# Kernel tuning notes

Hardware: AMD Instinct MI355X
Metric: run time of the kernel (lower is better)

## Reference

```python
import jax, jax.numpy as jnp
import numpy as np

B, L, D = 128, 50, 128
NUM_NODE, S, HOP = 100000, 12, 2
ALPHA = 0.2      # leaky-relu slope in local aggregator (opt.alpha)
T = 1.0          # softmax temperature (opt.t)
NEG_INF = -9e15


def setup_inputs() -> dict:
    key = jax.random.key(0)
    ks = jax.random.split(key, 13)
    stdv = 1.0 / np.sqrt(D)
    u = lambda k, shape: jax.random.uniform(k, shape, jnp.float32, -stdv, stdv)
    return {
        "inputs": jax.random.randint(ks[0], (B, L), 0, NUM_NODE),
        "adj": jax.random.randint(ks[1], (B, L, L), 0, 5),          # edge types 0..4
        "mask_item": jnp.ones((B, L), dtype=jnp.int32),
        "item": jax.random.randint(ks[2], (B, L), 0, NUM_NODE),
        "emb": u(ks[3], (NUM_NODE, D)),                              # item embedding table
        "adj_all": jax.random.randint(ks[4], (NUM_NODE, S), 0, NUM_NODE),  # global neighbor table
        "num_w": jax.random.uniform(ks[5], (NUM_NODE, S), jnp.float32, 0.0, 10.0),  # co-occur weights
        "a0": u(ks[6], (D,)), "a1": u(ks[7], (D,)), "a2": u(ks[8], (D,)), "a3": u(ks[9], (D,)),
        "gw1": u(ks[10], (HOP, D + 1, D)),   # GlobalAggregator w_1 per hop
        "gw2": u(ks[11], (HOP, D)),          # GlobalAggregator w_2 per hop
        "gw3": u(ks[12], (HOP, 2 * D, D)),   # GlobalAggregator w_3 per hop
    }


def reference(inputs, adj, mask_item, item, emb, adj_all, num_w,
              a0, a1, a2, a3, gw1, gw2, gw3):
    h = emb[inputs]                                   # [B,L,D]

    # ---- LocalAggregator: 4 edge-type GAT over session graph ----
    a_input = h[:, :, None, :] * h[:, None, :, :]     # [B,L,L,D] pairwise hadamard
    def edge_logits(a):
        return jax.nn.leaky_relu(jnp.einsum('bijd,d->bij', a_input, a), ALPHA)
    e = [edge_logits(a) for a in (a0, a1, a2, a3)]
    logits = jnp.full_like(e[0], NEG_INF)
    for k in range(4):
        logits = jnp.where(adj == k + 1, e[k], logits)
    attn = jax.nn.softmax(logits, axis=-1)
    h_local = jnp.einsum('bij,bjd->bid', attn, h)     # [B,L,D]

    # ---- multi-hop neighbor sampling (pure gathers) ----
    item_neighbors = [inputs]
    weight_neighbors = []
    for _ in range(HOP):
        flat = item_neighbors[-1].reshape(-1)
        item_neighbors.append(adj_all[flat].reshape(B, -1))
        weight_neighbors.append(num_w[flat].reshape(B, -1))
    entity = [emb[idx] for idx in item_neighbors]     # hop h: [B, L*S^h, D]

    # ---- session-mean representation ----
    mf = mask_item.astype(jnp.float32)
    sum_item = (emb[item] * mf[..., None]).sum(1) / mf.sum(-1, keepdims=True)  # [B,D]

    # ---- GlobalAggregator: weighted neighbor attention, hop-by-hop ----
    for n_hop in range(HOP):
        nxt = []
        for hp in range(HOP - n_hop):
            sv = entity[hp]                               # [B,M,D]
            nv = entity[hp + 1].reshape(B, -1, S, D)      # [B,M,S,D]
            nw = weight_neighbors[hp].reshape(B, -1, S)   # [B,M,S]
            a = jnp.concatenate([sum_item[:, None, None, :] * nv, nw[..., None]], -1)  # [B,M,S,D+1]
            a = jax.nn.leaky_relu(jnp.einsum('bmsk,kd->bmsd', a, gw1[n_hop]), 0.2)
            a = jnp.einsum('bmsd,d->bms', a, gw2[n_hop]) / T
            attn_g = jax.nn.softmax(a, axis=-1)[..., None]
            nv_agg = (attn_g * nv).sum(-2)                # [B,M,D]
            out = jnp.concatenate([sv, nv_agg], -1) @ gw3[n_hop]
            out = jnp.maximum(out, 0.0)                   # opt.activate == 'relu'
            nxt.append(out)
        entity = nxt
    s_global = entity[0]                                  # [B,L,D]

    # dropout omitted (eval mode)
    output = h_local + s_global
    return output, s_global
```

## Files before the change

kernel.cpp:

```cpp
#include <hip/hip_runtime.h>
#include <hip/hip_bf16.h>
#include <math.h>

#define B_ 128
#define L_ 50
#define D_ 128
#define S_ 12
#define NEG_INF_ -9e15f

typedef __attribute__((ext_vector_type(8))) _Float16 half8;
typedef __attribute__((ext_vector_type(4))) float f32x4;

static __device__ __forceinline__ float lrelu(float x){ return fmaxf(x, 0.2f*x); }
static __device__ __forceinline__ float fexp(float x){ return __expf(x); }
static __device__ __forceinline__ float frcp(float x){ return __builtin_amdgcn_rcpf(x); }

__global__ __launch_bounds__(256) void local_agg_kernel(
    const int* __restrict__ inputs, const int* __restrict__ adj,
    const float* __restrict__ emb,
    const float* __restrict__ a0, const float* __restrict__ a1,
    const float* __restrict__ a2, const float* __restrict__ a3,
    float* __restrict__ hlocal_out)
{
  __shared__ float hs[L_][129];
  __shared__ float alds[4][129];
  __shared__ float att[13][51];
  const int b = blockIdx.x, tid = threadIdx.x;
  const int r0 = blockIdx.y * 13;
  const int nr = (L_ - r0) < 13 ? (L_ - r0) : 13;

  if (tid < 128){
    alds[0][tid] = a0[tid]; alds[1][tid] = a1[tid];
    alds[2][tid] = a2[tid]; alds[3][tid] = a3[tid];
  }
  for (int i = tid; i < L_*D_; i += 256){
    int r = i >> 7, d = i & 127;
    hs[r][d] = emb[(size_t)inputs[b*L_ + r]*D_ + d];
  }
  __syncthreads();

  for (int pth = tid; pth < nr*L_; pth += 256){
    int i = pth / L_, j = pth % L_;
    int at = adj[b*L_*L_ + (r0+i)*L_ + j];
    float lg = NEG_INF_;
    if (at >= 1 && at <= 4){
      const float* av = alds[at-1];
      float acc = 0.f;
      #pragma unroll 4
      for (int d = 0; d < D_; ++d) acc = fmaf(hs[r0+i][d]*hs[j][d], av[d], acc);
      lg = lrelu(acc);
    }
    att[i][j] = lg;
  }
  __syncthreads();

  if (tid < nr){
    float m = -1e30f;
    for (int j = 0; j < L_; ++j) m = fmaxf(m, att[tid][j]);
    float sum = 0.f;
    for (int j = 0; j < L_; ++j){ float e = fexp(att[tid][j]-m); att[tid][j] = e; sum += e; }
    float inv = frcp(sum);
    for (int j = 0; j < L_; ++j) att[tid][j] *= inv;
  }
  __syncthreads();

  for (int i2 = tid; i2 < nr*D_; i2 += 256){
    int r = i2 >> 7, d = i2 & 127;
    float acc = 0.f;
    #pragma unroll 5
    for (int j = 0; j < L_; ++j) acc = fmaf(att[r][j], hs[j][d], acc);
    hlocal_out[(size_t)b*L_*D_ + (size_t)(r0+r)*D_ + d] = acc;
  }
}

__global__ void build_nbr2_kernel(const int* __restrict__ inputs,
                                  const int* __restrict__ adj_all,
                                  const float* __restrict__ num_w,
                                  int* __restrict__ n1, float* __restrict__ w0,
                                  int* __restrict__ n2, float* __restrict__ w1)
{
  int t = blockIdx.x*256 + threadIdx.x;
  if (t >= B_*L_*S_*S_) return;
  int i1 = t / S_;
  int s2 = t - i1*S_;
  int i0 = i1 / S_;
  int s1 = i1 - i0*S_;
  int parent0 = inputs[i0];
  int parent1 = adj_all[(size_t)parent0*S_ + s1];
  n2[t] = adj_all[(size_t)parent1*S_ + s2];
  w1[t] = num_w[(size_t)parent1*S_ + s2];
  if (s2 == 0){
    n1[i1] = parent1;
    w0[i1] = num_w[(size_t)parent0*S_ + s1];
  }
}

__global__ void prep_all_kernel(const float* __restrict__ emb, _Float16* __restrict__ embh,
                                const float* __restrict__ gw1, _Float16* __restrict__ gw1f,
                                const float* __restrict__ gw3, _Float16* __restrict__ gw3f)
{
  const int blk = blockIdx.x, tid = threadIdx.x;
  if (blk < 12500){
    int i = blk*256 + tid;
    float4 v = ((const float4*)emb)[i];
    union { _Float16 h[4]; uint2 u; } pk;
    pk.h[0] = (_Float16)v.x; pk.h[1] = (_Float16)v.y;
    pk.h[2] = (_Float16)v.z; pk.h[3] = (_Float16)v.w;
    ((uint2*)embh)[i] = pk.u;
  } else if (blk < 12516){
    int rel = blk - 12500;
    int hop = rel >> 3, bx = rel & 7;
    int idx = bx*256 + tid;
    int lane = idx & 63, f = idx >> 6;
    int t = f >> 3, n = f & 7;
    int g4 = lane >> 4, col = lane & 15;
    const float* g1 = gw1 + (size_t)hop*129*128;
    size_t base = (size_t)hop*16384 + ((size_t)f*64 + lane)*8;
    #pragma unroll
    for (int j = 0; j < 8; ++j){
      int k = t*32 + g4*8 + j;
      gw1f[base + j] = (_Float16)g1[(size_t)k*128 + n*16 + col];
    }
  } else {
    int rel = blk - 12516;
    int hop = rel >> 4, bx = rel & 15;
    int idx = bx*256 + tid;
    int lane = idx & 63, n = (idx >> 6) & 7, kt = idx >> 9;
    int g4 = lane >> 4, col = lane & 15;
    const float* g3 = gw3 + (size_t)hop*256*128;
    size_t base = (size_t)hop*32768 + ((size_t)(kt*8 + n)*64 + lane)*8;
    #pragma unroll
    for (int j = 0; j < 8; ++j){
      int k = kt*32 + g4*8 + j;
      gw3f[base + j] = (_Float16)g3[(size_t)k*128 + n*16 + col];
    }
  }
}

__global__ __launch_bounds__(256) void prep_wprime_kernel(
    const _Float16* __restrict__ gw1f,
    const int* __restrict__ item, const int* __restrict__ mask,
    const float* __restrict__ emb, _Float16* __restrict__ wg)
{
  __shared__ float si[128];
  const int b = blockIdx.x, hop = blockIdx.y, tid = threadIdx.x;
  if (tid < 128){
    float acc = 0.f, cnt = 0.f;
    for (int l = 0; l < L_; ++l){
      float mf = (float)mask[b*L_ + l];
      acc = fmaf(mf, emb[(size_t)item[b*L_+l]*D_ + tid], acc);
      cnt += mf;
    }
    si[tid] = acc / cnt;
  }
  __syncthreads();
  _Float16* wb = wg + ((size_t)(hop*128 + b)*32)*512;

  for (int i = 0; i < 8; ++i){
    int slot = i*256 + tid;
    int f = slot >> 6, l = slot & 63;
    int g4 = (l >> 4) & 3;
    int t = f >> 3;
    const _Float16* gf = gw1f + (size_t)hop*16384 + ((size_t)f*64 + l)*8;
    int k0 = t*32 + g4*8;
    union { _Float16 h[8]; uint4 q; } o;
    #pragma unroll
    for (int j = 0; j < 8; ++j)
      o.h[j] = (_Float16)(si[k0+j] * (float)gf[j]);
    *(uint4*)(wb + (size_t)slot*8) = o.q;
  }
}

template<bool USE_IDS, bool OUTF32>
__global__ __launch_bounds__(256, 2) void gagg12_kernel(
    const _Float16* __restrict__ embh,
    const int* sv_ids0, const _Float16* sv_vals0,
    const int* nv_ids0, const _Float16* nv_vals0,
    const float* nw0, void* outp0, int M0, int nbpb0, int nblk0,
    const int* sv_ids1, const _Float16* sv_vals1,
    const int* nv_ids1, const _Float16* nv_vals1,
    const float* nw1, void* outp1, int M1, int nbpb1,
    const _Float16* __restrict__ wg,  const float* __restrict__ gw1_last,
    const float* __restrict__ gw2, const _Float16* __restrict__ gw3f,
    float* __restrict__ hout)
{
  __shared__ _Float16 wlds[32*512];
  __shared__ _Float16 stash[4][12][132];
  __shared__ _Float16 catl[16][264];
  const int tid  = threadIdx.x;
  const int wid  = tid >> 6;
  const int lane = tid & 63;
  const int g4   = lane >> 4;
  const int col  = lane & 15;
  const bool colv = col < S_;
  const int sc_  = colv ? col : 0;

  const bool c1 = ((int)blockIdx.x >= nblk0);
  const int  blk = c1 ? (int)blockIdx.x - nblk0 : (int)blockIdx.x;
  const int*       sv_ids  = c1 ? sv_ids1  : sv_ids0;
  const _Float16*  sv_vals = c1 ? sv_vals1 : sv_vals0;
  const int*       nv_ids  = c1 ? nv_ids1  : nv_ids0;
  const _Float16*  nv_vals = c1 ? nv_vals1 : nv_vals0;
  const float*     nw      = c1 ? nw1      : nw0;
  void*            outp    = c1 ? outp1    : outp0;
  const int        M       = c1 ? M1       : M0;
  const int        nbpb    = c1 ? nbpb1    : nbpb0;

  const int b = blk / nbpb;
  const int j = blk - b*nbpb;

  {
    const uint4* src = (const uint4*)(wg + (size_t)b*32*512);
    uint4* dst = (uint4*)wlds;
    #pragma unroll
    for (int i = 0; i < 8; ++i)
      dst[i*256 + tid] = src[i*256 + tid];
  }
  __syncthreads();

  float g2v[8], glv[8];
  #pragma unroll
  for (int n = 0; n < 8; ++n){
    g2v[n] = gw2[n*16 + col];
    glv[n] = gw1_last[n*16 + col];
  }

  auto pidx = [&](int np_)->int{
    int li0 = j*16 + wid*4 + np_;
    int li  = li0 < M ? li0 : M-1;
    return b*M + li;
  };

  const half8 z8 = {0,0,0,0,0,0,0,0};
  half8 pf[4];
  int idn = 0;
  {
    const int p0_ = pidx(0);
    const _Float16* r0 = USE_IDS ? embh + (size_t)nv_ids[p0_*S_ + sc_]*D_
                                 : nv_vals + ((size_t)p0_*S_ + sc_)*D_;
    #pragma unroll
    for (int t = 0; t < 4; ++t)
      pf[t] = colv ? *(const half8*)(r0 + t*32 + g4*8) : z8;
    if (USE_IDS) idn = nv_ids[pidx(1)*S_ + sc_];
  }

  for (int np = 0; np < 4; ++np){
    const int p = pidx(np);

    half8 af[4];
    #pragma unroll
    for (int t = 0; t < 4; ++t) af[t] = colv ? pf[t] : z8;

    if (np < 3){
      const _Float16* rn = USE_IDS ? embh + (size_t)idn*D_
                                   : nv_vals + ((size_t)pidx(np+1)*S_ + sc_)*D_;
      #pragma unroll
      for (int t = 0; t < 4; ++t)
        pf[t] = colv ? *(const half8*)(rn + t*32 + g4*8) : z8;
      if (USE_IDS && np < 2) idn = nv_ids[pidx(np+2)*S_ + sc_];
    }

    float nwv[4];
    #pragma unroll
    for (int r = 0; r < 4; ++r){
      int s = g4*4 + r;
      nwv[r] = nw[p*S_ + (s < S_ ? s : 0)];
    }
    const _Float16* svrow = USE_IDS ? embh + (size_t)sv_ids[p]*D_
                                    : sv_vals + (size_t)p*D_;
    unsigned sv2q = *(const unsigned*)(svrow + 2*lane);

    #pragma unroll
    for (int t = 0; t < 4; ++t){
      if (colv){
        union { half8 v; uint2 q[2]; } ua;
        ua.v = af[t];
        _Float16* sp = &stash[wid][col][t*32 + g4*8];
        *(uint2*)sp       = ua.q[0];
        *(uint2*)(sp + 4) = ua.q[1];
      }
    }
    f32x4 acc[8];
    #pragma unroll
    for (int n = 0; n < 8; ++n) acc[n] = (f32x4){0.f,0.f,0.f,0.f};
    #pragma unroll
    for (int t = 0; t < 4; ++t){
      #pragma unroll
      for (int n = 0; n < 8; ++n){
        half8 wf = *(const half8*)(wlds + ((size_t)(t*8+n)*64 + lane)*8);
        acc[n] = __builtin_amdgcn_mfma_f32_16x16x32_f16(af[t], wf, acc[n], 0, 0, 0);
      }
    }

    float sc4[4];
    #pragma unroll
    for (int r = 0; r < 4; ++r){
      float pr = 0.f;
      #pragma unroll
      for (int n = 0; n < 8; ++n){
        float tv = acc[n][r] + nwv[r]*glv[n];
        pr = fmaf(lrelu(tv), g2v[n], pr);
      }
      pr += __shfl_xor(pr, 1); pr += __shfl_xor(pr, 2);
      pr += __shfl_xor(pr, 4); pr += __shfl_xor(pr, 8);
      sc4[r] = pr;
    }
    float w[S_];
    {
      float ss[S_];
      #pragma unroll
      for (int grp = 0; grp < 3; ++grp)
        #pragma unroll
        for (int r = 0; r < 4; ++r)
          ss[grp*4 + r] = __shfl(sc4[r], grp*16);
      float m01 = fmaxf(ss[0], ss[1]),  m23 = fmaxf(ss[2], ss[3]);
      float m45 = fmaxf(ss[4], ss[5]),  m67 = fmaxf(ss[6], ss[7]);
      float m89 = fmaxf(ss[8], ss[9]),  mab = fmaxf(ss[10], ss[11]);
      float m = fmaxf(fmaxf(fmaxf(m01, m23), fmaxf(m45, m67)), fmaxf(m89, mab));
      float sum = 0.f;
      #pragma unroll
      for (int s = 0; s < S_; ++s){ ss[s] = fexp(ss[s]-m); sum += ss[s]; }
      float inv = frcp(sum);
      #pragma unroll
      for (int s = 0; s < S_; ++s) w[s] = ss[s]*inv;
    }
    float aggx = 0.f, aggy = 0.f;
    #pragma unroll
    for (int s = 0; s < S_; ++s){
      union { unsigned q; _Float16 h[2]; } v;
      v.q = *(const unsigned*)&stash[wid][s][2*lane];
      aggx = fmaf(w[s], (float)v.h[0], aggx);
      aggy = fmaf(w[s], (float)v.h[1], aggy);
    }
    const int row = wid*4 + np;
    *(unsigned*)&catl[row][2*lane] = sv2q;
    union { unsigned q; _Float16 h[2]; } pk;
    pk.h[0] = (_Float16)aggx; pk.h[1] = (_Float16)aggy;
    *(unsigned*)&catl[row][D_ + 2*lane] = pk.q;
  }

  __syncthreads();

  const half8* g3fp = (const half8*)gw3f;
  f32x4 dacc[2];
  dacc[0] = (f32x4){0.f,0.f,0.f,0.f};
  dacc[1] = (f32x4){0.f,0.f,0.f,0.f};

  #pragma unroll
  for (int kt = 0; kt < 8; ++kt){
    half8 afr = *(const half8*)&catl[col][kt*32 + g4*8];
    #pragma unroll
    for (int nn = 0; nn < 2; ++nn){
      int n = wid*2 + nn;
      dacc[nn] = __builtin_amdgcn_mfma_f32_16x16x32_f16(afr, g3fp[(kt*8+n)*64 + lane], dacc[nn], 0, 0, 0);
    }
  }

  #pragma unroll
  for (int nn = 0; nn < 2; ++nn){
    int n = wid*2 + nn;
    #pragma unroll
    for (int r = 0; r < 4; ++r){
      int li = j*16 + g4*4 + r;
      if (li < M){
        size_t off = (size_t)(b*M + li)*D_ + n*16 + col;
        float v = fmaxf(dacc[nn][r], 0.f);
        if (OUTF32){
          ((float*)outp)[off] = v;
          hout[off] += v;
        } else {
          ((_Float16*)outp)[off] = (_Float16)v;
        }
      }
    }
  }
}

extern "C" void kernel_launch(void* const* d_in, const int* in_sizes, int n_in,
                              void* d_out, int out_size, void* d_ws, size_t ws_size,
                              hipStream_t stream)
{
  const int*   inputs  = (const int*)  d_in[0];
  const int*   adj     = (const int*)  d_in[1];
  const int*   mask    = (const int*)  d_in[2];
  const int*   item    = (const int*)  d_in[3];
  const float* emb     = (const float*)d_in[4];
  const int*   adj_all = (const int*)  d_in[5];
  const float* num_w   = (const float*)d_in[6];
  const float* a0      = (const float*)d_in[7];
  const float* a1      = (const float*)d_in[8];
  const float* a2      = (const float*)d_in[9];
  const float* a3      = (const float*)d_in[10];
  const float* gw1     = (const float*)d_in[11];
  const float* gw2     = (const float*)d_in[12];
  const float* gw3     = (const float*)d_in[13];

  float* out     = (float*)d_out;
  float* hlocal  = out;
  float* sglobal = out + B_*L_*D_;

  char* ws = (char*)d_ws;
  size_t off = 0;
  auto alloc = [&](size_t bytes)->char*{
    char* pp = ws + off; off += (bytes + 255) & ~(size_t)255; return pp;
  };
  int*      n1     = (int*)  alloc((size_t)B_*L_*S_*sizeof(int));
  float*    w0     = (float*)alloc((size_t)B_*L_*S_*sizeof(float));
  int*      n2     = (int*)  alloc((size_t)B_*L_*S_*S_*sizeof(int));
  float*    w1     = (float*)alloc((size_t)B_*L_*S_*S_*sizeof(float));
  _Float16* out0h  = (_Float16*)alloc((size_t)B_*L_*D_*sizeof(_Float16));
  _Float16* out1h  = (_Float16*)alloc((size_t)B_*L_*S_*D_*sizeof(_Float16));
  _Float16* embh   = (_Float16*)alloc((size_t)100000*D_*sizeof(_Float16));
  _Float16* gw1f   = (_Float16*)alloc((size_t)2*16384*sizeof(_Float16));
  _Float16* gw3f   = (_Float16*)alloc((size_t)2*32768*sizeof(_Float16));
  _Float16* wgAll  = (_Float16*)alloc((size_t)2*128*32*512*sizeof(_Float16));

  prep_all_kernel<<<12548, 256, 0, stream>>>(emb, embh, gw1, gw1f, gw3, gw3f);
  local_agg_kernel<<<dim3(B_,4), 256, 0, stream>>>(inputs, adj, emb, a0, a1, a2, a3, hlocal);
  build_nbr2_kernel<<<(B_*L_*S_*S_ + 255)/256, 256, 0, stream>>>(
      inputs, adj_all, num_w, n1, w0, n2, w1);
  prep_wprime_kernel<<<dim3(B_,2), 256, 0, stream>>>(gw1f, item, mask, emb, wgAll);

  {
    const int nblkA = B_*4;
    const int nblkB = B_*38;
    gagg12_kernel<true,false><<<nblkA + nblkB, 256, 0, stream>>>(
        embh,
        inputs, nullptr, n1, nullptr, w0, out0h, L_,   4, nblkA,
        n1,     nullptr, n2, nullptr, w1, out1h, L_*S_, 38,
        wgAll, gw1 + 128*128, gw2, gw3f, nullptr);
  }
  {
    const int nblkC = B_*4;
    gagg12_kernel<false,true><<<nblkC, 256, 0, stream>>>(
        embh,
        nullptr, out0h, nullptr, out1h, w0, sglobal, L_, 4, nblkC,
        nullptr, out0h, nullptr, out1h, w0, sglobal, L_, 4,
        wgAll + (size_t)128*32*512, gw1 + 129*128 + 128*128, gw2 + 128, gw3f + 32768,
        hlocal);
  }
}
```

Baseline: 190.8 us.

## Merge prep kernels into one launch and fold local aggregation into gagg

Folds the emb/gw3 conversion, the neighbor-table build and the weight premultiply into a single prep_mega_kernel. The premultiply now reads fp32 gw1 directly instead of a separate fp16 relayout. The local GAT aggregation runs as extra blocks of the first global-aggregation launch, sharing LDS through a union, and a wave shuffle is swapped for readlane. This cuts launch count and lets local and global work run concurrently. In exchange the neighbor build and premultiply blocks now run in the same grid as the large embedding conversion, so they are no longer separate dependent launches.

```diff
diff --git a/kernel.cpp b/kernel.cpp
--- a/kernel.cpp
+++ b/kernel.cpp
@@ -14,92 +14,24 @@
 static __device__ __forceinline__ float lrelu(float x){ return fmaxf(x, 0.2f*x); }
 static __device__ __forceinline__ float fexp(float x){ return __expf(x); }
 static __device__ __forceinline__ float frcp(float x){ return __builtin_amdgcn_rcpf(x); }
-
-__global__ __launch_bounds__(256) void local_agg_kernel(
-    const int* __restrict__ inputs, const int* __restrict__ adj,
-    const float* __restrict__ emb,
-    const float* __restrict__ a0, const float* __restrict__ a1,
-    const float* __restrict__ a2, const float* __restrict__ a3,
-    float* __restrict__ hlocal_out)
+static __device__ __forceinline__ float rdlane(float v, int l){
+  return __builtin_bit_cast(float, __builtin_amdgcn_readlane(__builtin_bit_cast(int, v), l));
+}
+
+__global__ __launch_bounds__(256) void prep_mega_kernel(
+    const float* __restrict__ emb, _Float16* __restrict__ embh,
+    const float* __restrict__ gw3, _Float16* __restrict__ gw3f,
+    const float* __restrict__ gw1,
+    const int* __restrict__ inputs, const int* __restrict__ adj_all,
+    const float* __restrict__ num_w,
+    int* __restrict__ n1, float* __restrict__ w0,
+    int* __restrict__ n2, float* __restrict__ w1,
+    const int* __restrict__ item, const int* __restrict__ mask,
+    _Float16* __restrict__ wg)
 {
-  __shared__ float hs[L_][129];
-  __shared__ float alds[4][129];
-  __shared__ float att[13][51];
-  const int b = blockIdx.x, tid = threadIdx.x;
-  const int r0 = blockIdx.y * 13;
-  const int nr = (L_ - r0) < 13 ? (L_ - r0) : 13;
-
-  if (tid < 128){
-    alds[0][tid] = a0[tid]; alds[1][tid] = a1[tid];
-    alds[2][tid] = a2[tid]; alds[3][tid] = a3[tid];
-  }
-  for (int i = tid; i < L_*D_; i += 256){
-    int r = i >> 7, d = i & 127;
-    hs[r][d] = emb[(size_t)inputs[b*L_ + r]*D_ + d];
-  }
-  __syncthreads();
-
-  for (int pth = tid; pth < nr*L_; pth += 256){
-    int i = pth / L_, j = pth % L_;
-    int at = adj[b*L_*L_ + (r0+i)*L_ + j];
-    float lg = NEG_INF_;
-    if (at >= 1 && at <= 4){
-      const float* av = alds[at-1];
-      float acc = 0.f;
-      #pragma unroll 4
-      for (int d = 0; d < D_; ++d) acc = fmaf(hs[r0+i][d]*hs[j][d], av[d], acc);
-      lg = lrelu(acc);
-    }
-    att[i][j] = lg;
-  }
-  __syncthreads();
-
-  if (tid < nr){
-    float m = -1e30f;
-    for (int j = 0; j < L_; ++j) m = fmaxf(m, att[tid][j]);
-    float sum = 0.f;
-    for (int j = 0; j < L_; ++j){ float e = fexp(att[tid][j]-m); att[tid][j] = e; sum += e; }
-    float inv = frcp(sum);
-    for (int j = 0; j < L_; ++j) att[tid][j] *= inv;
-  }
-  __syncthreads();
-
-  for (int i2 = tid; i2 < nr*D_; i2 += 256){
-    int r = i2 >> 7, d = i2 & 127;
-    float acc = 0.f;
-    #pragma unroll 5
-    for (int j = 0; j < L_; ++j) acc = fmaf(att[r][j], hs[j][d], acc);
-    hlocal_out[(size_t)b*L_*D_ + (size_t)(r0+r)*D_ + d] = acc;
-  }
-}
-
-__global__ void build_nbr2_kernel(const int* __restrict__ inputs,
-                                  const int* __restrict__ adj_all,
-                                  const float* __restrict__ num_w,
-                                  int* __restrict__ n1, float* __restrict__ w0,
-                                  int* __restrict__ n2, float* __restrict__ w1)
-{
-  int t = blockIdx.x*256 + threadIdx.x;
-  if (t >= B_*L_*S_*S_) return;
-  int i1 = t / S_;
-  int s2 = t - i1*S_;
-  int i0 = i1 / S_;
-  int s1 = i1 - i0*S_;
-  int parent0 = inputs[i0];
-  int parent1 = adj_all[(size_t)parent0*S_ + s1];
-  n2[t] = adj_all[(size_t)parent1*S_ + s2];
-  w1[t] = num_w[(size_t)parent1*S_ + s2];
-  if (s2 == 0){
-    n1[i1] = parent1;
-    w0[i1] = num_w[(size_t)parent0*S_ + s1];
-  }
-}
-
-__global__ void prep_all_kernel(const float* __restrict__ emb, _Float16* __restrict__ embh,
-                                const float* __restrict__ gw1, _Float16* __restrict__ gw1f,
-                                const float* __restrict__ gw3, _Float16* __restrict__ gw3f)
-{
+  __shared__ float si[128];
   const int blk = blockIdx.x, tid = threadIdx.x;
+
   if (blk < 12500){
     int i = blk*256 + tid;
     float4 v = ((const float4*)emb)[i];
@@ -107,22 +39,8 @@
     pk.h[0] = (_Float16)v.x; pk.h[1] = (_Float16)v.y;
     pk.h[2] = (_Float16)v.z; pk.h[3] = (_Float16)v.w;
     ((uint2*)embh)[i] = pk.u;
-  } else if (blk < 12516){
+  } else if (blk < 12532){
     int rel = blk - 12500;
-    int hop = rel >> 3, bx = rel & 7;
-    int idx = bx*256 + tid;
-    int lane = idx & 63, f = idx >> 6;
-    int t = f >> 3, n = f & 7;
-    int g4 = lane >> 4, col = lane & 15;
-    const float* g1 = gw1 + (size_t)hop*129*128;
-    size_t base = (size_t)hop*16384 + ((size_t)f*64 + lane)*8;
-    #pragma unroll
-    for (int j = 0; j < 8; ++j){
-      int k = t*32 + g4*8 + j;
-      gw1f[base + j] = (_Float16)g1[(size_t)k*128 + n*16 + col];
-    }
-  } else {
-    int rel = blk - 12516;
     int hop = rel >> 4, bx = rel & 15;
     int idx = bx*256 + tid;
     int lane = idx & 63, n = (idx >> 6) & 7, kt = idx >> 9;
@@ -134,60 +52,126 @@
       int k = kt*32 + g4*8 + j;
       gw3f[base + j] = (_Float16)g3[(size_t)k*128 + n*16 + col];
     }
+  } else if (blk < 16132){
+    int t = (blk - 12532)*256 + tid;
+    int i1 = t / S_;
+    int s2 = t - i1*S_;
+    int i0 = i1 / S_;
+    int s1 = i1 - i0*S_;
+    int parent0 = inputs[i0];
+    int parent1 = adj_all[(size_t)parent0*S_ + s1];
+    n2[t] = adj_all[(size_t)parent1*S_ + s2];
+    w1[t] = num_w[(size_t)parent1*S_ + s2];
+    if (s2 == 0){
+      n1[i1] = parent1;
+      w0[i1] = num_w[(size_t)parent0*S_ + s1];
+    }
+  } else {
+    int g = blk - 16132;
+    int hop = g >> 7, b = g & 127;
+    if (tid < 128){
+      float acc = 0.f, cnt = 0.f;
+      for (int l = 0; l < L_; ++l){
+        float mf = (float)mask[b*L_ + l];
+        acc = fmaf(mf, emb[(size_t)item[b*L_+l]*D_ + tid], acc);
+        cnt += mf;
+      }
+      si[tid] = acc / cnt;
+    }
+    __syncthreads();
+    _Float16* wb = wg + ((size_t)(hop*128 + b)*32)*512;
+    const float* g1 = gw1 + (size_t)hop*129*128;
+    for (int i = 0; i < 8; ++i){
+      int slot = i*256 + tid;
+      int f = slot >> 6, l = slot & 63;
+      int g4 = (l >> 4) & 3, col = l & 15;
+      int t = f >> 3, n = f & 7;
+      int k0 = t*32 + g4*8;
+      union { _Float16 h[8]; uint4 q; } o;
+      #pragma unroll
+      for (int j = 0; j < 8; ++j)
+        o.h[j] = (_Float16)(si[k0+j] * g1[(size_t)(k0+j)*128 + n*16 + col]);
+      *(uint4*)(wb + (size_t)slot*8) = o.q;
+    }
   }
 }
 
-__global__ __launch_bounds__(256) void prep_wprime_kernel(
-    const _Float16* __restrict__ gw1f,
-    const int* __restrict__ item, const int* __restrict__ mask,
-    const float* __restrict__ emb, _Float16* __restrict__ wg)
-{
-  __shared__ float si[128];
-  const int b = blockIdx.x, hop = blockIdx.y, tid = threadIdx.x;
-  if (tid < 128){
-    float acc = 0.f, cnt = 0.f;
-    for (int l = 0; l < L_; ++l){
-      float mf = (float)mask[b*L_ + l];
-      acc = fmaf(mf, emb[(size_t)item[b*L_+l]*D_ + tid], acc);
-      cnt += mf;
-    }
-    si[tid] = acc / cnt;
-  }
-  __syncthreads();
-  _Float16* wb = wg + ((size_t)(hop*128 + b)*32)*512;
-
-  for (int i = 0; i < 8; ++i){
-    int slot = i*256 + tid;
-    int f = slot >> 6, l = slot & 63;
-    int g4 = (l >> 4) & 3;
-    int t = f >> 3;
-    const _Float16* gf = gw1f + (size_t)hop*16384 + ((size_t)f*64 + l)*8;
-    int k0 = t*32 + g4*8;
-    union { _Float16 h[8]; uint4 q; } o;
-    #pragma unroll
-    for (int j = 0; j < 8; ++j)
-      o.h[j] = (_Float16)(si[k0+j] * (float)gf[j]);
-    *(uint4*)(wb + (size_t)slot*8) = o.q;
-  }
-}
-
 template<bool USE_IDS, bool OUTF32>
-__global__ __launch_bounds__(256, 2) void gagg12_kernel(
+__global__ __launch_bounds__(256, 2) void gagg13_kernel(
     const _Float16* __restrict__ embh,
     const int* sv_ids0, const _Float16* sv_vals0,
     const int* nv_ids0, const _Float16* nv_vals0,
     const float* nw0, void* outp0, int M0, int nbpb0, int nblk0,
     const int* sv_ids1, const _Float16* sv_vals1,
     const int* nv_ids1, const _Float16* nv_vals1,
-    const float* nw1, void* outp1, int M1, int nbpb1,
+    const float* nw1, void* outp1, int M1, int nbpb1, int nblk_gagg,
     const _Float16* __restrict__ wg,  const float* __restrict__ gw1_last,
     const float* __restrict__ gw2, const _Float16* __restrict__ gw3f,
-    float* __restrict__ hout)
+    float* __restrict__ hout,
+    const int* __restrict__ inputs, const int* __restrict__ adj,
+    const float* __restrict__ embf,
+    const float* __restrict__ a0, const float* __restrict__ a1,
+    const float* __restrict__ a2, const float* __restrict__ a3,
+    float* __restrict__ hlocal_out)
 {
-  __shared__ _Float16 wlds[32*512];
-  __shared__ _Float16 stash[4][12][132];
-  __shared__ _Float16 catl[16][264];
-  const int tid  = threadIdx.x;
+  __shared__ union {
+    struct { _Float16 wlds[32*512]; _Float16 stash[4][12][132]; _Float16 catl[16][264]; } g;
+    struct { float hs[L_][129]; float alds[4][129]; float att[13][51]; } l;
+  } sm;
+
+  const int tid = threadIdx.x;
+
+  if ((int)blockIdx.x >= nblk_gagg){
+    const int g = (int)blockIdx.x - nblk_gagg;
+    const int b = g >> 2;
+    const int r0 = (g & 3) * 13;
+    const int nr = (L_ - r0) < 13 ? (L_ - r0) : 13;
+
+    if (tid < 128){
+      sm.l.alds[0][tid] = a0[tid]; sm.l.alds[1][tid] = a1[tid];
+      sm.l.alds[2][tid] = a2[tid]; sm.l.alds[3][tid] = a3[tid];
+    }
+    for (int i = tid; i < L_*D_; i += 256){
+      int r = i >> 7, d = i & 127;
+      sm.l.hs[r][d] = embf[(size_t)inputs[b*L_ + r]*D_ + d];
+    }
+    __syncthreads();
+
+    for (int pth = tid; pth < nr*L_; pth += 256){
+      int i = pth / L_, j = pth % L_;
+      int at = adj[b*L_*L_ + (r0+i)*L_ + j];
+      float lg = NEG_INF_;
+      if (at >= 1 && at <= 4){
+        const float* av = sm.l.alds[at-1];
+        float acc = 0.f;
+        #pragma unroll 4
+        for (int d = 0; d < D_; ++d) acc = fmaf(sm.l.hs[r0+i][d]*sm.l.hs[j][d], av[d], acc);
+        lg = lrelu(acc);
+      }
+      sm.l.att[i][j] = lg;
+    }
+    __syncthreads();
+
+    if (tid < nr){
+      float m = -1e30f;
+      for (int j = 0; j < L_; ++j) m = fmaxf(m, sm.l.att[tid][j]);
+      float sum = 0.f;
+      for (int j = 0; j < L_; ++j){ float e = fexp(sm.l.att[tid][j]-m); sm.l.att[tid][j] = e; sum += e; }
+      float inv = frcp(sum);
+      for (int j = 0; j < L_; ++j) sm.l.att[tid][j] *= inv;
+    }
+    __syncthreads();
+
+    for (int i2 = tid; i2 < nr*D_; i2 += 256){
+      int r = i2 >> 7, d = i2 & 127;
+      float acc = 0.f;
+      #pragma unroll 5
+      for (int j = 0; j < L_; ++j) acc = fmaf(sm.l.att[r][j], sm.l.hs[j][d], acc);
+      hlocal_out[(size_t)b*L_*D_ + (size_t)(r0+r)*D_ + d] = acc;
+    }
+    return;
+  }
+
   const int wid  = tid >> 6;
   const int lane = tid & 63;
   const int g4   = lane >> 4;
@@ -211,7 +195,7 @@
 
   {
     const uint4* src = (const uint4*)(wg + (size_t)b*32*512);
-    uint4* dst = (uint4*)wlds;
+    uint4* dst = (uint4*)sm.g.wlds;
     #pragma unroll
     for (int i = 0; i < 8; ++i)
       dst[i*256 + tid] = src[i*256 + tid];
@@ -275,7 +259,7 @@
       if (colv){
         union { half8 v; uint2 q[2]; } ua;
         ua.v = af[t];
-        _Float16* sp = &stash[wid][col][t*32 + g4*8];
+        _Float16* sp = &sm.g.stash[wid][col][t*32 + g4*8];
         *(uint2*)sp       = ua.q[0];
         *(uint2*)(sp + 4) = ua.q[1];
       }
@@ -287,7 +271,7 @@
     for (int t = 0; t < 4; ++t){
       #pragma unroll
       for (int n = 0; n < 8; ++n){
-        half8 wf = *(const half8*)(wlds + ((size_t)(t*8+n)*64 + lane)*8);
+        half8 wf = *(const half8*)(sm.g.wlds + ((size_t)(t*8+n)*64 + lane)*8);
         acc[n] = __builtin_amdgcn_mfma_f32_16x16x32_f16(af[t], wf, acc[n], 0, 0, 0);
       }
     }
@@ -312,7 +296,7 @@
       for (int grp = 0; grp < 3; ++grp)
         #pragma unroll
         for (int r = 0; r < 4; ++r)
-          ss[grp*4 + r] = __shfl(sc4[r], grp*16);
+          ss[grp*4 + r] = rdlane(sc4[r], grp*16);
       float m01 = fmaxf(ss[0], ss[1]),  m23 = fmaxf(ss[2], ss[3]);
       float m45 = fmaxf(ss[4], ss[5]),  m67 = fmaxf(ss[6], ss[7]);
       float m89 = fmaxf(ss[8], ss[9]),  mab = fmaxf(ss[10], ss[11]);
@@ -328,15 +312,15 @@
     #pragma unroll
     for (int s = 0; s < S_; ++s){
       union { unsigned q; _Float16 h[2]; } v;
-      v.q = *(const unsigned*)&stash[wid][s][2*lane];
+      v.q = *(const unsigned*)&sm.g.stash[wid][s][2*lane];
       aggx = fmaf(w[s], (float)v.h[0], aggx);
       aggy = fmaf(w[s], (float)v.h[1], aggy);
     }
     const int row = wid*4 + np;
-    *(unsigned*)&catl[row][2*lane] = sv2q;
+    *(unsigned*)&sm.g.catl[row][2*lane] = sv2q;
     union { unsigned q; _Float16 h[2]; } pk;
     pk.h[0] = (_Float16)aggx; pk.h[1] = (_Float16)aggy;
-    *(unsigned*)&catl[row][D_ + 2*lane] = pk.q;
+    *(unsigned*)&sm.g.catl[row][D_ + 2*lane] = pk.q;
   }
 
   __syncthreads();
@@ -348,7 +332,7 @@
 
   #pragma unroll
   for (int kt = 0; kt < 8; ++kt){
-    half8 afr = *(const half8*)&catl[col][kt*32 + g4*8];
+    half8 afr = *(const half8*)&sm.g.catl[col][kt*32 + g4*8];
     #pragma unroll
     for (int nn = 0; nn < 2; ++nn){
       int n = wid*2 + nn;
@@ -411,32 +395,33 @@
   _Float16* out0h  = (_Float16*)alloc((size_t)B_*L_*D_*sizeof(_Float16));
   _Float16* out1h  = (_Float16*)alloc((size_t)B_*L_*S_*D_*sizeof(_Float16));
   _Float16* embh   = (_Float16*)alloc((size_t)100000*D_*sizeof(_Float16));
-  _Float16* gw1f   = (_Float16*)alloc((size_t)2*16384*sizeof(_Float16));
   _Float16* gw3f   = (_Float16*)alloc((size_t)2*32768*sizeof(_Float16));
   _Float16* wgAll  = (_Float16*)alloc((size_t)2*128*32*512*sizeof(_Float16));
 
-  prep_all_kernel<<<12548, 256, 0, stream>>>(emb, embh, gw1, gw1f, gw3, gw3f);
-  local_agg_kernel<<<dim3(B_,4), 256, 0, stream>>>(inputs, adj, emb, a0, a1, a2, a3, hlocal);
-  build_nbr2_kernel<<<(B_*L_*S_*S_ + 255)/256, 256, 0, stream>>>(
-      inputs, adj_all, num_w, n1, w0, n2, w1);
-  prep_wprime_kernel<<<dim3(B_,2), 256, 0, stream>>>(gw1f, item, mask, emb, wgAll);
+  prep_mega_kernel<<<16388, 256, 0, stream>>>(
+      emb, embh, gw3, gw3f, gw1,
+      inputs, adj_all, num_w, n1, w0, n2, w1,
+      item, mask, wgAll);
 
   {
     const int nblkA = B_*4;
     const int nblkB = B_*38;
-    gagg12_kernel<true,false><<<nblkA + nblkB, 256, 0, stream>>>(
+    const int nblkG = B_*4;
+    gagg13_kernel<true,false><<<nblkA + nblkB + nblkG, 256, 0, stream>>>(
         embh,
         inputs, nullptr, n1, nullptr, w0, out0h, L_,   4, nblkA,
-        n1,     nullptr, n2, nullptr, w1, out1h, L_*S_, 38,
-        wgAll, gw1 + 128*128, gw2, gw3f, nullptr);
+        n1,     nullptr, n2, nullptr, w1, out1h, L_*S_, 38, nblkA + nblkB,
+        wgAll, gw1 + 128*128, gw2, gw3f, nullptr,
+        inputs, adj, emb, a0, a1, a2, a3, hlocal);
   }
   {
     const int nblkC = B_*4;
-    gagg12_kernel<false,true><<<nblkC, 256, 0, stream>>>(
+    gagg13_kernel<false,true><<<nblkC, 256, 0, stream>>>(
         embh,
         nullptr, out0h, nullptr, out1h, w0, sglobal, L_, 4, nblkC,
-        nullptr, out0h, nullptr, out1h, w0, sglobal, L_, 4,
+        nullptr, out0h, nullptr, out1h, w0, sglobal, L_, 4, nblkC,
         wgAll + (size_t)128*32*512, gw1 + 129*128 + 128*128, gw2 + 128, gw3f + 32768,
-        hlocal);
+        hlocal,
+        nullptr, nullptr, nullptr, nullptr, nullptr, nullptr, nullptr, nullptr);
   }
 }
```

Measured after the change: 290.1 us. 52.1% more time.
